# Optimization experiments

Hardware: AMD Instinct MI355X
Metric: run time of the kernel (lower is better)

The kernel has to match this reference:

```python
import jax, jax.numpy as jnp
import numpy as np

B, N, C = 16384, 4, 512
H = 8
HD = C // H
WIN = 2
SCALE = HD ** -0.5
HID = 2048


def _rel_pos_index(w):
    # same construction as the torch buffer, done in numpy (constant)
    coords = np.stack(np.meshgrid(np.arange(w), np.arange(w), indexing='ij'))  # [2,w,w]
    flat = coords.reshape(2, -1)                      # [2, w*w]
    rel = flat[:, :, None] - flat[:, None, :]         # [2, N, N]
    rel = rel.transpose(1, 2, 0).astype(np.int64)     # [N, N, 2]
    rel[:, :, 0] += w - 1
    rel[:, :, 1] += w - 1
    rel[:, :, 0] *= 2 * w - 1
    return rel.sum(-1)                                # [N, N]

REL_IDX = _rel_pos_index(WIN)


def setup_inputs() -> dict:
    key = jax.random.key(0)
    ks = jax.random.split(key, 8)
    s = lambda fan: 1.0 / np.sqrt(fan)
    return {
        'x': jax.random.normal(ks[0], (B, N, C), jnp.float32),
        'ln_g': jnp.ones((C,), jnp.float32),
        'ln_b': jnp.zeros((C,), jnp.float32),
        'qkv_w': jax.random.normal(ks[1], (3 * C, C), jnp.float32) * s(C),
        'proj_w': jax.random.normal(ks[2], (C, C), jnp.float32) * s(C),
        'proj_b': jnp.zeros((C,), jnp.float32),
        'rpb_table': jax.random.normal(ks[3], ((2 * WIN - 1) ** 2, H), jnp.float32) * 0.02,
        'fc1_w': jax.random.normal(ks[4], (HID, C), jnp.float32) * s(C),
        'fc1_b': jnp.zeros((HID,), jnp.float32),
        'fc2_w': jax.random.normal(ks[5], (C, HID), jnp.float32) * s(HID),
        'fc2_b': jnp.zeros((C,), jnp.float32),
    }


def _layernorm(x, g, b, eps=1e-5):
    mu = jnp.mean(x, axis=-1, keepdims=True)
    var = jnp.mean(jnp.square(x - mu), axis=-1, keepdims=True)
    return (x - mu) * jax.lax.rsqrt(var + eps) * g + b


def reference(x, ln_g, ln_b, qkv_w, proj_w, proj_b, rpb_table, fc1_w, fc1_b, fc2_w, fc2_b):
    # --- attention branch (pre-norm, shared LayerNorm params) ---
    h = _layernorm(x, ln_g, ln_b)
    qkv = h @ qkv_w.T                                  # [B,N,3C]
    qkv = qkv.reshape(B, N, 3, H, HD).transpose(2, 0, 3, 1, 4)  # [3,B,H,N,HD]
    q, k, v = qkv[0], qkv[1], qkv[2]
    attn = jnp.einsum('bhnd,bhmd->bhnm', q, k) * SCALE  # [B,H,N,N]
    bias = rpb_table[REL_IDX.reshape(-1)].reshape(N, N, H).transpose(2, 0, 1)  # [H,N,N]
    attn = jax.nn.softmax(attn + bias[None], axis=-1)
    o = jnp.einsum('bhnm,bhmd->bhnd', attn, v)          # [B,H,N,HD]
    o = o.transpose(0, 2, 1, 3).reshape(B, N, C)
    o = o @ proj_w.T + proj_b
    x = x + o
    # --- MLP branch (same LayerNorm params reused, as in the torch code) ---
    h = _layernorm(x, ln_g, ln_b)
    h = jax.nn.gelu(h @ fc1_w.T + fc1_b, approximate=False)
    h = h @ fc2_w.T + fc2_b
    return x + h
```

## Files before the change

### kernel.cpp

```cpp
#include <hip/hip_runtime.h>
#include <hip/hip_bf16.h>
#include <math.h>

#define BQ   16384
#define CH   512
#define NH   8
#define HID  2048
#define NTOK (BQ*4)

using bf16 = __hip_bfloat16;
typedef __bf16 bf16x8 __attribute__((ext_vector_type(8)));
typedef float  f32x4  __attribute__((ext_vector_type(4)));

#define FENCE() asm volatile("" ::: "memory")

__device__ __forceinline__ void gload16(const void* g, void* l) {
    __builtin_amdgcn_global_load_lds(
        (const __attribute__((address_space(1))) void*)g,
        (__attribute__((address_space(3))) void*)l, 16, 0, 0);
}

__device__ __forceinline__ void packw_one(const float* Wsrc, bf16* out, int q, int K) {
    int NSk = K >> 5;
    int l  = q & 63;
    int jj = (q >> 6) & 1;
    int w  = (q >> 7) & 3;
    int s  = (q >> 9) % NSk;
    int cb = q / (NSk * 512);
    int row = cb * 128 + w * 32 + jj * 16 + (l >> 2);
    int k   = s * 32 + ((l & 3) ^ ((l >> 3) & 3)) * 8;
    const float* src = Wsrc + (size_t)row * K + k;
    float4 v0 = *(const float4*)src;
    float4 v1 = *(const float4*)(src + 4);
    __align__(16) bf16 t[8];
    t[0] = __float2bfloat16(v0.x); t[1] = __float2bfloat16(v0.y);
    t[2] = __float2bfloat16(v0.z); t[3] = __float2bfloat16(v0.w);
    t[4] = __float2bfloat16(v1.x); t[5] = __float2bfloat16(v1.y);
    t[6] = __float2bfloat16(v1.z); t[7] = __float2bfloat16(v1.w);
    *(uint4*)&out[(size_t)q * 8] = *(const uint4*)t;
}

__global__ __launch_bounds__(256)
void packall(const float* qkv_w, const float* proj_w,
             const float* fc1_w, const float* fc2_w,
             bf16* wQKV, bf16* wPROJ, bf16* wFC1, bf16* wFC2) {
    int q = blockIdx.x * 256 + threadIdx.x;
    if (q < 98304)            packw_one(qkv_w,  wQKV,  q,           512);
    else if (q < 131072)      packw_one(proj_w, wPROJ, q - 98304,   512);
    else if (q < 262144)      packw_one(fc1_w,  wFC1,  q - 131072,  512);
    else                      packw_one(fc2_w,  wFC2,  q - 262144, 2048);
}

template<int BF16IN>
__global__ __launch_bounds__(256) void ln_kernel(const void* __restrict__ xin,
                                                 const float* __restrict__ g,
                                                 const float* __restrict__ b,
                                                 bf16* __restrict__ out) {
    int row  = blockIdx.x * 4 + (threadIdx.x >> 6);
    int lane = threadIdx.x & 63;
    int c0 = lane * 8;
    float f[8];
    if (BF16IN) {
        const bf16* xr = (const bf16*)xin + (size_t)row * CH;
        union { uint4 u4; bf16 h[8]; } uu;
        uu.u4 = *(const uint4*)&xr[c0];
#pragma unroll
        for (int i = 0; i < 8; ++i) f[i] = __bfloat162float(uu.h[i]);
    } else {
        const float* xr = (const float*)xin + (size_t)row * CH;
        float4 v0 = *(const float4*)&xr[c0];
        float4 v1 = *(const float4*)&xr[c0 + 4];
        f[0]=v0.x; f[1]=v0.y; f[2]=v0.z; f[3]=v0.w;
        f[4]=v1.x; f[5]=v1.y; f[6]=v1.z; f[7]=v1.w;
    }
    float s = 0.f, sq = 0.f;
#pragma unroll
    for (int i = 0; i < 8; ++i) { s += f[i]; sq += f[i] * f[i]; }
#pragma unroll
    for (int off = 32; off >= 1; off >>= 1) {
        s  += __shfl_xor(s,  off, 64);
        sq += __shfl_xor(sq, off, 64);
    }
    float mu  = s * (1.0f / CH);
    float var = sq * (1.0f / CH) - mu * mu;
    float rs  = rsqrtf(var + 1e-5f);
    float4 g0 = *(const float4*)&g[c0];
    float4 g1 = *(const float4*)&g[c0 + 4];
    float4 b0 = *(const float4*)&b[c0];
    float4 b1 = *(const float4*)&b[c0 + 4];
    float gg[8] = {g0.x,g0.y,g0.z,g0.w,g1.x,g1.y,g1.z,g1.w};
    float bb[8] = {b0.x,b0.y,b0.z,b0.w,b1.x,b1.y,b1.z,b1.w};
    __align__(16) bf16 t[8];
#pragma unroll
    for (int i = 0; i < 8; ++i)
        t[i] = __float2bfloat16((f[i] - mu) * rs * gg[i] + bb[i]);
    *(uint4*)&out[(size_t)row * CH + c0] = *(const uint4*)t;
}

template<int EPI>
__global__ __launch_bounds__(512, 4)
void gemm256x128(const bf16* __restrict__ A, const bf16* __restrict__ Bp,
                 int M, int N, int K, int nbx,
                 const float* __restrict__ bias,
                 const float* residF, const bf16* residB,
                 float* outF, bf16* __restrict__ outB) {
    __shared__ __align__(16) char lds[49152];
    const int tid  = threadIdx.x;
    const int w    = tid >> 6;
    const int lane = tid & 63;

    const int nb  = gridDim.x;
    const int id  = blockIdx.x;
    const int swz = (id & 7) * (nb >> 3) + (id >> 3);
    const int bx  = swz % nbx, by = swz / nbx;
    const int bm = by * 256, bn = bx * 128;
    const int wrq = w >> 1;
    const int wch = w & 1;
    const int NSk = K >> 5;

    const int rl  = lane >> 2;
    const int kpe = ((lane & 3) ^ ((lane >> 3) & 3)) * 8;
    const bf16* gA0 = A + (size_t)(bm + w * 32 + rl) * K + kpe;
    const bf16* gA1 = gA0 + (size_t)16 * K;
    const bf16* gB = Bp + (size_t)(bn >> 7) * NSk * 4096 + w * 512 + lane * 8;

    const int kslot = ((lane >> 4) ^ ((lane >> 1) & 3));
    const int aoff = (wrq * 64 + (lane & 15)) * 64 + kslot * 16;
    const int boff = 16384 + (wch * 64 + (lane & 15)) * 64 + kslot * 16;

    f32x4 acc[4][4] = {};

    auto stage = [&](int s) {
        char* base = (char*)lds + (s & 1) * 24576;
        gload16(gA0 + (size_t)s * 32, base + w * 2048);
        gload16(gA1 + (size_t)s * 32, base + w * 2048 + 1024);
        gload16(gB  + (size_t)s * 4096, base + 16384 + w * 1024);
    };

    auto compute = [&](int slot) {
        const char* base = (const char*)lds + slot * 24576;
        bf16x8 av[4], bv[4];
#pragma unroll
        for (int n = 0; n < 4; ++n)
            bv[n] = *(const bf16x8*)(base + boff + n * 1024);
#pragma unroll
        for (int m = 0; m < 4; ++m)
            av[m] = *(const bf16x8*)(base + aoff + m * 1024);
#pragma unroll
        for (int m = 0; m < 4; ++m)
#pragma unroll
            for (int n = 0; n < 4; ++n)
                acc[m][n] = __builtin_amdgcn_mfma_f32_16x16x32_bf16(av[m], bv[n], acc[m][n], 0, 0, 0);
    };

#define WAITV(n) asm volatile("s_waitcnt vmcnt(" #n ")" ::: "memory")

    stage(0);
    for (int s = 0; s < NSk - 1; ++s) {
        stage(s + 1);
        WAITV(3);
        __builtin_amdgcn_s_barrier();
        FENCE();
        compute(s & 1);
        FENCE();
        __builtin_amdgcn_s_barrier();
    }
    WAITV(0);
    __builtin_amdgcn_s_barrier();
    FENCE();
    compute((NSk - 1) & 1);
#undef WAITV

    const int erow0 = bm + wrq * 64 + (lane >> 4) * 4;
    const int ecol0 = bn + wch * 64 + (lane & 15);
#pragma unroll
    for (int m = 0; m < 4; ++m) {
#pragma unroll
        for (int n = 0; n < 4; ++n) {
            int col = ecol0 + n * 16;
#pragma unroll
            for (int r = 0; r < 4; ++r) {
                int row = erow0 + m * 16 + r;
                size_t idx = (size_t)row * N + col;
                float v = acc[m][n][r];
                if (EPI == 0) {
                    outB[idx] = __float2bfloat16(v);
                } else if (EPI == 1) {
                    outF[idx] = v + bias[col] + residF[idx];
                } else if (EPI == 2) {
                    float t = v + bias[col];
                    float u2 = 1.5957691216f * t * (1.0f + 0.044715f * t * t);
                    float e = __expf(u2);
                    float rcp = __builtin_amdgcn_rcpf(e + 1.0f);
                    outB[idx] = __float2bfloat16(t - t * rcp);
                } else if (EPI == 3) {
                    outB[idx] = __float2bfloat16(v + bias[col] + residF[idx]);
                } else {
                    outF[idx] = v + bias[col] + __bfloat162float(residB[idx]);
                }
            }
        }
    }
}

__global__ __launch_bounds__(256)
void attn_kernel(const bf16* __restrict__ qkv, const float* __restrict__ rpb,
                 bf16* __restrict__ o) {
    __shared__ __align__(16) bf16 sT[4 * 1536];
    __shared__ float sS[NH][4][4];
    __shared__ float sP[NH][4][4];
    int b   = blockIdx.x;
    int tid = threadIdx.x;
    const bf16* src = qkv + (size_t)b * (4 * 1536);
#pragma unroll
    for (int it = 0; it < 3; ++it) {
        int e = (it * 256 + tid) * 8;
        *(uint4*)&sT[e] = *(const uint4*)&src[e];
    }
    __syncthreads();
    if (tid < 128) {
        int h = tid >> 4, i = (tid >> 2) & 3, j = tid & 3;
        const bf16* q = &sT[i * 1536 + h * 64];
        const bf16* k = &sT[j * 1536 + 512 + h * 64];
        float acc = 0.f;
#pragma unroll
        for (int d = 0; d < 64; ++d)
            acc += __bfloat162float(q[d]) * __bfloat162float(k[d]);
        int rel = (((i >> 1) - (j >> 1)) + 1) * 3 + (((i & 1) - (j & 1)) + 1);
        sS[h][i][j] = acc * 0.125f + rpb[rel * NH + h];
    }
    __syncthreads();
    if (tid < 32) {
        int h = tid >> 2, i = tid & 3;
        float s0 = sS[h][i][0], s1 = sS[h][i][1], s2 = sS[h][i][2], s3 = sS[h][i][3];
        float mx = fmaxf(fmaxf(s0, s1), fmaxf(s2, s3));
        float e0 = expf(s0 - mx), e1 = expf(s1 - mx), e2 = expf(s2 - mx), e3 = expf(s3 - mx);
        float inv = 1.f / (e0 + e1 + e2 + e3);
        sP[h][i][0] = e0 * inv; sP[h][i][1] = e1 * inv;
        sP[h][i][2] = e2 * inv; sP[h][i][3] = e3 * inv;
    }
    __syncthreads();
    {
        int h = tid >> 5, tl = tid & 31;
        int d = tl * 2;
        const bf16* v = &sT[1024 + h * 64 + d];
#pragma unroll
        for (int i = 0; i < 4; ++i) {
            float p0 = sP[h][i][0], p1 = sP[h][i][1], p2 = sP[h][i][2], p3 = sP[h][i][3];
            float o0 = p0 * __bfloat162float(v[0])        + p1 * __bfloat162float(v[1536])
                     + p2 * __bfloat162float(v[2 * 1536]) + p3 * __bfloat162float(v[3 * 1536]);
            float o1 = p0 * __bfloat162float(v[1])            + p1 * __bfloat162float(v[1536 + 1])
                     + p2 * __bfloat162float(v[2 * 1536 + 1]) + p3 * __bfloat162float(v[3 * 1536 + 1]);
            __hip_bfloat162 pr;
            pr.x = __float2bfloat16(o0);
            pr.y = __float2bfloat16(o1);
            *(__hip_bfloat162*)&o[(size_t)(b * 4 + i) * CH + h * 64 + d] = pr;
        }
    }
}

extern "C" void kernel_launch(void* const* d_in, const int* in_sizes, int n_in,
                              void* d_out, int out_size, void* d_ws, size_t ws_size,
                              hipStream_t stream) {
    const float* x      = (const float*)d_in[0];
    const float* ln_g   = (const float*)d_in[1];
    const float* ln_b   = (const float*)d_in[2];
    const float* qkv_w  = (const float*)d_in[3];
    const float* proj_w = (const float*)d_in[4];
    const float* proj_b = (const float*)d_in[5];
    const float* rpb    = (const float*)d_in[6];
    const float* fc1_w  = (const float*)d_in[7];
    const float* fc1_b  = (const float*)d_in[8];
    const float* fc2_w  = (const float*)d_in[9];
    const float* fc2_b  = (const float*)d_in[10];
    float* out = (float*)d_out;

    char* ws = (char*)d_ws;
    bf16* wQKV  = (bf16*)ws;  ws += (size_t)1536 * 512 * 2;
    bf16* wPROJ = (bf16*)ws;  ws += (size_t)512  * 512 * 2;
    bf16* wFC1  = (bf16*)ws;  ws += (size_t)2048 * 512 * 2;
    bf16* wFC2  = (bf16*)ws;  ws += (size_t)512 * 2048 * 2;
    bf16* hA    = (bf16*)ws;  ws += (size_t)NTOK * 512 * 2;
    bf16* big   = (bf16*)ws;  ws += (size_t)NTOK * 2048 * 2;
    bf16* x1b   = (bf16*)ws;
    const size_t needed  = 6291456ull + 67108864ull + 268435456ull;
    const size_t needed2 = needed + 67108864ull;
    if (ws_size < needed) return;
    const bool useb = (ws_size >= needed2);

    packall<<<1536, 256, 0, stream>>>(qkv_w, proj_w, fc1_w, fc2_w,
                                      wQKV, wPROJ, wFC1, wFC2);

    ln_kernel<0><<<NTOK / 4, 256, 0, stream>>>(x, ln_g, ln_b, hA);
    gemm256x128<0><<<dim3(256 * 12), 512, 0, stream>>>(
        hA, wQKV, NTOK, 1536, 512, 12, nullptr, nullptr, nullptr, nullptr, big);
    attn_kernel<<<BQ, 256, 0, stream>>>(big, rpb, hA);

    if (useb) {
        gemm256x128<3><<<dim3(256 * 4), 512, 0, stream>>>(
            hA, wPROJ, NTOK, 512, 512, 4, proj_b, x, nullptr, nullptr, x1b);
        ln_kernel<1><<<NTOK / 4, 256, 0, stream>>>(x1b, ln_g, ln_b, hA);
        gemm256x128<2><<<dim3(256 * 16), 512, 0, stream>>>(
            hA, wFC1, NTOK, 2048, 512, 16, fc1_b, nullptr, nullptr, nullptr, big);
        gemm256x128<4><<<dim3(256 * 4), 512, 0, stream>>>(
            big, wFC2, NTOK, 512, 2048, 4, fc2_b, nullptr, x1b, out, nullptr);
    } else {
        gemm256x128<1><<<dim3(256 * 4), 512, 0, stream>>>(
            hA, wPROJ, NTOK, 512, 512, 4, proj_b, x, nullptr, out, nullptr);
        ln_kernel<0><<<NTOK / 4, 256, 0, stream>>>(out, ln_g, ln_b, hA);
        gemm256x128<2><<<dim3(256 * 16), 512, 0, stream>>>(
            hA, wFC1, NTOK, 2048, 512, 16, fc1_b, nullptr, nullptr, nullptr, big);
        gemm256x128<1><<<dim3(256 * 4), 512, 0, stream>>>(
            big, wFC2, NTOK, 512, 2048, 4, fc2_b, out, nullptr, out, nullptr);
    }
}
```

Baseline: 738.7 us.

## Add 256x256 K64 GEMM kernel with finer-grained pipelining for FC2

Adds a new GEMM kernel for the FC2 projection (K=2048) that uses 256x256 output tiles, 64-wide K steps and 128KB of double-buffered LDS. It interleaves sub-tile LDS reads, next-stage global-to-LDS loads and MFMA groups with priority raising. FC2 weights are repacked into a matching XOR-swizzled 64-wide layout. The aim is more data reuse per tile and better overlap of loads with compute on the longest-K GEMM, at the cost of lower occupancy (2 blocks per CU) and a grid of only 512 blocks.

```diff
diff --git a/kernel.cpp b/kernel.cpp
--- a/kernel.cpp
+++ b/kernel.cpp
@@ -40,6 +40,26 @@
     *(uint4*)&out[(size_t)q * 8] = *(const uint4*)t;
 }
 
+__device__ __forceinline__ void pack64_one(const float* Wsrc, bf16* out, int q, int K) {
+    int NKT = K >> 6;
+    int j  = q & 7;
+    int r  = (q >> 3) & 127;
+    int h  = (q >> 10) & 1;
+    int kt = (q >> 11) % NKT;
+    int cb = q / (NKT << 11);
+    int row = cb * 256 + h * 128 + r;
+    int col = kt * 64 + (j ^ (r & 7)) * 8;
+    const float* src = Wsrc + (size_t)row * K + col;
+    float4 v0 = *(const float4*)src;
+    float4 v1 = *(const float4*)(src + 4);
+    __align__(16) bf16 t[8];
+    t[0] = __float2bfloat16(v0.x); t[1] = __float2bfloat16(v0.y);
+    t[2] = __float2bfloat16(v0.z); t[3] = __float2bfloat16(v0.w);
+    t[4] = __float2bfloat16(v1.x); t[5] = __float2bfloat16(v1.y);
+    t[6] = __float2bfloat16(v1.z); t[7] = __float2bfloat16(v1.w);
+    *(uint4*)&out[(size_t)q * 8] = *(const uint4*)t;
+}
+
 __global__ __launch_bounds__(256)
 void packall(const float* qkv_w, const float* proj_w,
              const float* fc1_w, const float* fc2_w,
@@ -48,7 +68,7 @@
     if (q < 98304)            packw_one(qkv_w,  wQKV,  q,           512);
     else if (q < 131072)      packw_one(proj_w, wPROJ, q - 98304,   512);
     else if (q < 262144)      packw_one(fc1_w,  wFC1,  q - 131072,  512);
-    else                      packw_one(fc2_w,  wFC2,  q - 262144, 2048);
+    else                      pack64_one(fc2_w, wFC2,  q - 262144, 2048);
 }
 
 template<int BF16IN>
@@ -108,7 +128,6 @@
     const int tid  = threadIdx.x;
     const int w    = tid >> 6;
     const int lane = tid & 63;
-
     const int nb  = gridDim.x;
     const int id  = blockIdx.x;
     const int swz = (id & 7) * (nb >> 3) + (id >> 3);
@@ -154,7 +173,6 @@
     };
 
 #define WAITV(n) asm volatile("s_waitcnt vmcnt(" #n ")" ::: "memory")
-
     stage(0);
     for (int s = 0; s < NSk - 1; ++s) {
         stage(s + 1);
@@ -203,6 +221,140 @@
     }
 }
 
+template<int EPI>
+__global__ __launch_bounds__(512, 2)
+void gemm64(const bf16* __restrict__ A, const bf16* __restrict__ Bp,
+            int M, int N, int K, int nbx,
+            const float* __restrict__ bias,
+            const float* residF, const bf16* residB,
+            float* outF, bf16* __restrict__ outB) {
+    __shared__ __align__(16) char lds[131072];
+    const int tid  = threadIdx.x;
+    const int w    = tid >> 6;
+    const int lane = tid & 63;
+
+    const int nb  = gridDim.x;
+    const int id  = blockIdx.x;
+    const int swz = (id & 7) * (nb >> 3) + (id >> 3);
+    const int bx  = swz % nbx, by = swz / nbx;
+    const int bm = by * 256, bn = bx * 256;
+    const int wr = w >> 2;
+    const int wc = w & 3;
+    const int NT = K >> 6;
+
+    const bf16* gA0 = A + (size_t)(bm + w * 16 + (lane >> 3)) * K
+                        + ((lane & 7) ^ ((lane >> 3) & 7)) * 8;
+    const bf16* gB0 = Bp + (size_t)(bn >> 8) * NT * 16384 + w * 1024 + lane * 8;
+
+    const int abase_off = wr * 16384 + (lane & 15) * 128;
+    const int bbase_off = 32768 + (wc >> 1) * 16384 + ((wc & 1) * 64 + (lane & 15)) * 128;
+    const int aj0 = (((lane >> 4)    ) ^ (lane & 7)) * 16;
+    const int aj1 = (((lane >> 4) + 4) ^ (lane & 7)) * 16;
+
+    f32x4 acc[8][4] = {};
+    bf16x8 av[4][2], bv[2][2], bw[2][2];
+
+    auto stA = [&](int X, int ah) {
+        char* d = (char*)lds + (X & 1) * 65536 + ah * 16384 + w * 2048;
+        const bf16* s = gA0 + (size_t)ah * 128 * K + (size_t)X * 64;
+        gload16(s, d);
+        gload16(s + (size_t)8 * K, d + 1024);
+    };
+    auto stB = [&](int X, int bh) {
+        char* d = (char*)lds + (X & 1) * 65536 + 32768 + bh * 16384 + w * 2048;
+        const bf16* s = gB0 + ((size_t)X * 2 + bh) * 8192;
+        gload16(s, d);
+        gload16(s + 512, d + 1024);
+    };
+
+#define RD_A(MH) { const char* _p = bb + abase_off + (MH) * 8192;            \
+    _Pragma("unroll") for (int _m = 0; _m < 4; ++_m) {                       \
+        av[_m][0] = *(const bf16x8*)(_p + _m * 2048 + aj0);                  \
+        av[_m][1] = *(const bf16x8*)(_p + _m * 2048 + aj1); } }
+#define RD_B(BV, NB) { const char* _p = bb + bbase_off + (NB) * 2048;        \
+    BV[0][0] = *(const bf16x8*)(_p + aj0);                                   \
+    BV[0][1] = *(const bf16x8*)(_p + aj1);                                   \
+    BV[1][0] = *(const bf16x8*)(_p + 2048 + aj0);                            \
+    BV[1][1] = *(const bf16x8*)(_p + 2048 + aj1); }
+#define MQ(BV, MB, NB) { __builtin_amdgcn_s_setprio(1);                      \
+    _Pragma("unroll") for (int _m = 0; _m < 4; ++_m)                         \
+    _Pragma("unroll") for (int _n = 0; _n < 2; ++_n) {                       \
+        acc[(MB)+_m][(NB)+_n] = __builtin_amdgcn_mfma_f32_16x16x32_bf16(     \
+            av[_m][0], BV[_n][0], acc[(MB)+_m][(NB)+_n], 0, 0, 0);           \
+        acc[(MB)+_m][(NB)+_n] = __builtin_amdgcn_mfma_f32_16x16x32_bf16(     \
+            av[_m][1], BV[_n][1], acc[(MB)+_m][(NB)+_n], 0, 0, 0); }         \
+    __builtin_amdgcn_s_setprio(0); }
+#define WAITV2() asm volatile("s_waitcnt vmcnt(2)" ::: "memory")
+#define WAITV0() asm volatile("s_waitcnt vmcnt(0)" ::: "memory")
+#define SBAR()   __builtin_amdgcn_s_barrier()
+#define LGKM0()  asm volatile("s_waitcnt lgkmcnt(0)" ::: "memory")
+
+#define ITER_BODY(T, DO_ST1, DO_ST2, TAILW)                                  \
+    { const char* bb = (const char*)lds + ((T) & 1) * 65536;                 \
+                                                                    \
+      RD_A(0); RD_B(bv, 0); FENCE();                                        \
+      if (DO_ST1) stA((T) + 1, 1);                                           \
+      SBAR(); LGKM0(); MQ(bv, 0, 0); SBAR();                                 \
+                                                                    \
+      RD_B(bw, 2); FENCE();                                                  \
+      if (DO_ST1) stB((T) + 1, 0);                                           \
+      SBAR(); LGKM0(); MQ(bw, 0, 2); SBAR();                                 \
+                                                                    \
+      RD_A(1); FENCE();                                                      \
+      if (DO_ST1) stB((T) + 1, 1);                                           \
+      SBAR(); LGKM0(); MQ(bv, 4, 0); SBAR();                                 \
+                                                                    \
+      if (DO_ST2) stA((T) + 2, 0);                                           \
+      MQ(bw, 4, 2);                                                          \
+      TAILW; SBAR(); }
+
+    stA(0, 0); stA(0, 1); stB(0, 0); stB(0, 1); stA(1, 0);
+    WAITV2(); SBAR();
+
+    for (int t = 0; t < NT - 2; ++t)
+        ITER_BODY(t, true, true, WAITV2())
+    ITER_BODY(NT - 2, true, false, WAITV0())
+    {
+        const char* bb = (const char*)lds + ((NT - 1) & 1) * 65536;
+        RD_A(0); RD_B(bv, 0); FENCE();
+        SBAR(); LGKM0(); MQ(bv, 0, 0); SBAR();
+        RD_B(bw, 2); FENCE();
+        SBAR(); LGKM0(); MQ(bw, 0, 2); SBAR();
+        RD_A(1); FENCE();
+        SBAR(); LGKM0(); MQ(bv, 4, 0); SBAR();
+        MQ(bw, 4, 2);
+    }
+#undef RD_A
+#undef RD_B
+#undef MQ
+#undef WAITV2
+#undef WAITV0
+#undef SBAR
+#undef LGKM0
+#undef ITER_BODY
+
+    const int erow0 = bm + wr * 128 + (lane >> 4) * 4;
+    const int ecol0 = bn + wc * 64 + (lane & 15);
+#pragma unroll
+    for (int m = 0; m < 8; ++m) {
+#pragma unroll
+        for (int n = 0; n < 4; ++n) {
+            int col = ecol0 + n * 16;
+#pragma unroll
+            for (int r = 0; r < 4; ++r) {
+                int row = erow0 + m * 16 + r;
+                size_t idx = (size_t)row * N + col;
+                float v = acc[m][n][r];
+                if (EPI == 1) {
+                    outF[idx] = v + bias[col] + residF[idx];
+                } else {
+                    outF[idx] = v + bias[col] + __bfloat162float(residB[idx]);
+                }
+            }
+        }
+    }
+}
+
 __global__ __launch_bounds__(256)
 void attn_kernel(const bf16* __restrict__ qkv, const float* __restrict__ rpb,
                  bf16* __restrict__ o) {
@@ -302,15 +454,15 @@
         ln_kernel<1><<<NTOK / 4, 256, 0, stream>>>(x1b, ln_g, ln_b, hA);
         gemm256x128<2><<<dim3(256 * 16), 512, 0, stream>>>(
             hA, wFC1, NTOK, 2048, 512, 16, fc1_b, nullptr, nullptr, nullptr, big);
-        gemm256x128<4><<<dim3(256 * 4), 512, 0, stream>>>(
-            big, wFC2, NTOK, 512, 2048, 4, fc2_b, nullptr, x1b, out, nullptr);
+        gemm64<4><<<dim3(256 * 2), 512, 0, stream>>>(
+            big, wFC2, NTOK, 512, 2048, 2, fc2_b, nullptr, x1b, out, nullptr);
     } else {
         gemm256x128<1><<<dim3(256 * 4), 512, 0, stream>>>(
             hA, wPROJ, NTOK, 512, 512, 4, proj_b, x, nullptr, out, nullptr);
         ln_kernel<0><<<NTOK / 4, 256, 0, stream>>>(out, ln_g, ln_b, hA);
         gemm256x128<2><<<dim3(256 * 16), 512, 0, stream>>>(
             hA, wFC1, NTOK, 2048, 512, 16, fc1_b, nullptr, nullptr, nullptr, big);
-        gemm256x128<1><<<dim3(256 * 4), 512, 0, stream>>>(
-            big, wFC2, NTOK, 512, 2048, 4, fc2_b, out, nullptr, out, nullptr);
-    }
-}
+        gemm64<1><<<dim3(256 * 2), 512, 0, stream>>>(
+            big, wFC2, NTOK, 512, 2048, 2, fc2_b, out, nullptr, out, nullptr);
+    }
+}
```

Measured after the change: 730.1 us. Within noise of the previous version (-1.2%).
